# Kernel optimization log

Hardware: AMD Instinct MI355X
Metric: run time of the kernel (lower is better)

The kernel has to match this reference:

```python
import jax, jax.numpy as jnp
import numpy as np

CDIM = 32
SCALES = (1, 16, 64, 256, 1024, 4096)  # last entry == T
INV_TEMP = 100.0
ENT_W = 0.1
COMMIT_W = 0.2
Q_SCALE = 1.0 / float(np.sqrt(CDIM))


def _interp_area(x, pt):
    # x: [B, T, C] -> [B, pt, C]; T divisible by pt so 'area' == block mean
    B, T, C = x.shape
    return x.reshape(B, pt, T // pt, C).mean(axis=2)


def _interp_linear(x, T):
    # x: [B, pt, C] -> [B, T, C]; mode='linear', align_corners=False
    pt = x.shape[1]
    pos = (jnp.arange(T, dtype=jnp.float32) + 0.5) * (pt / T) - 0.5
    pos = jnp.clip(pos, 0.0, pt - 1.0)
    lo = jnp.floor(pos).astype(jnp.int32)
    hi = jnp.minimum(lo + 1, pt - 1)
    w = (pos - lo.astype(jnp.float32))[None, :, None]
    return x[:, lo] * (1.0 - w) + x[:, hi] * w


def _bsq(f):
    # L2 normalize (torch F.normalize: clamp_min on norm)
    f = f / jnp.maximum(jnp.linalg.norm(f, axis=-1, keepdims=True), 1e-12)
    # sign quantize with STE
    zhat = jnp.where(f > 0, Q_SCALE, -Q_SCALE).astype(f.dtype)
    quantized = f + jax.lax.stop_gradient(zhat - f)
    # soft entropy loss
    p = jax.nn.sigmoid(-4.0 * f * (INV_TEMP / float(np.sqrt(CDIM))))
    prob = jnp.stack([p, 1.0 - p], axis=-1)  # [B, T, C, 2]
    ent = lambda c: -(c * jnp.log(c + 1e-8)).sum(axis=-1)
    per_sample_entropy = ent(prob).sum(axis=-1).mean()
    avg_prob = prob.mean(axis=(0, 1))  # [C, 2]
    cb_entropy = ent(avg_prob).sum()
    entropy_penalty = (per_sample_entropy - cb_entropy) / INV_TEMP
    commit = ((jax.lax.stop_gradient(quantized) - f) ** 2).sum(axis=-1).mean()
    aux = entropy_penalty * ENT_W + commit * COMMIT_W
    bits = (quantized > 0).astype(jnp.int32)
    return quantized, bits, aux


def setup_inputs() -> dict:
    key = jax.random.key(0)
    B, T, C = 128, SCALES[-1], CDIM
    return {"f_BTC": jax.random.normal(key, (B, T, C), dtype=jnp.float32)}


def reference(f_BTC):
    B, T, C = f_BTC.shape
    quantized_out = jnp.zeros_like(f_BTC)
    residual = f_BTC
    losses, bit_list = [], []
    for pt in SCALES:
        interp_res = _interp_area(residual, pt) if pt != T else residual
        q, bits, loss = _bsq(interp_res)
        q = _interp_linear(q, T) if pt != T else q
        residual = residual - jax.lax.stop_gradient(q)
        quantized_out = quantized_out + q
        bit_list.append(bits)
        losses.append(loss)
    all_losses = jnp.stack(losses, axis=-1)       # [num_scales]
    all_bits = jnp.concatenate(bit_list, axis=1)  # [B, sum(SCALES), C]
    return quantized_out, all_bits, all_losses
```

## Files before the change

kernel.cpp:

```cpp
#include <hip/hip_runtime.h>
#include <hip/hip_bf16.h>
#include <cstddef>
#include <cstdint>

#define NB 128
#define NT 4096
#define NC 32
#define BITROWS 5457
#define QV_ROWS 1361
#define QOUT_ELEMS (NB*NT*NC)
#define BITS_ELEMS (NB*BITROWS*NC)

#define ACC_OFF  22298624
#define S16_OFF  22302720

__device__ __constant__ float kQSC = 0.17677669529663687f;
__device__ __constant__ float kSIG = 17.67766952966369f;

__device__ __forceinline__ float interp_slice(const float* __restrict__ q, int P, int base, int t, int c) {
  float pos = ((float)t + 0.5f) * ((float)P * (1.0f / 4096.0f)) - 0.5f;
  pos = fminf(fmaxf(pos, 0.0f), (float)(P - 1));
  const int lo = (int)pos;
  const int hi = min(lo + 1, P - 1);
  const float w = pos - (float)lo;
  const float a = __fmul_rn(q[(lo - base) * NC + c], 1.0f - w);
  const float b = __fmul_rn(q[(hi - base) * NC + c], w);
  return __fadd_rn(a, b);
}

__device__ __forceinline__ float interp_w(const float* __restrict__ plo, const float* __restrict__ phi, float w) {
  const float a = __fmul_rn(*plo, 1.0f - w);
  const float b = __fmul_rn(*phi, w);
  return __fadd_rn(a, b);
}

__device__ __forceinline__ void process_elem(
    float msum, float invn, int b, int rowOff, int j, int c,
    float* qlsRow, float* __restrict__ qvG, float* __restrict__ bitsG,
    float& entA, float& comA, float& pA)
{
  const float m = msum * invn;
  float ss = m * m;
  #pragma unroll
  for (int mk = 16; mk; mk >>= 1) ss += __shfl_xor(ss, mk, 32);
  const float den = fmaxf(sqrtf(ss), 1e-12f);
  const float fn = m / den;
  const bool bit = fn > 0.0f;
  const float zh = bit ? kQSC : -kQSC;
  const float qvv = fn + (zh - fn);
  if (qlsRow) qlsRow[c] = qvv;
  if (qvG) qvG[(size_t)b * (QV_ROWS * NC) + (size_t)(rowOff + j) * NC + c] = qvv;
  bitsG[(size_t)b * (BITROWS * NC) + (size_t)(rowOff + j) * NC + c] = bit ? 1.0f : 0.0f;
  const float arg = (-4.0f * fn) * kSIG;
  const float p = 1.0f / (1.0f + __expf(-arg));
  const float ent = -(p * __logf(p + 1e-8f) + (1.0f - p) * __logf((1.0f - p) + 1e-8f));
  const float d = qvv - fn;
  entA += ent; comA += d * d; pA += p;
}

__device__ __forceinline__ float quant_silent(float msum, float invn) {
  const float m = msum * invn;
  float ss = m * m;
  #pragma unroll
  for (int mk = 16; mk; mk >>= 1) ss += __shfl_xor(ss, mk, 32);
  const float den = fmaxf(sqrtf(ss), 1e-12f);
  const float fn = m / den;
  const float zh = (fn > 0.0f) ? kQSC : -kQSC;
  return fn + (zh - fn);
}

__device__ __forceinline__ void reduce_losses(
    int sIdx, float entA, float comA, float pA, int tid, int nWaves,
    double* __restrict__ acc, float* redE, float* redC, float* redP)
{
  float e = entA, cm = comA;
  #pragma unroll
  for (int mk = 32; mk; mk >>= 1) { e += __shfl_xor(e, mk, 64); cm += __shfl_xor(cm, mk, 64); }
  const float p = pA + __shfl_xor(pA, 32, 64);
  const int w = tid >> 6, lane = tid & 63;
  if (lane == 0) { redE[w] = e; redC[w] = cm; }
  if (lane < 32) redP[w * 32 + lane] = p;
  __syncthreads();
  if (tid == 0) {
    double te = 0.0, tc = 0.0;
    for (int i = 0; i < nWaves; ++i) { te += (double)redE[i]; tc += (double)redC[i]; }
    atomicAdd(&acc[sIdx], te);
    atomicAdd(&acc[6 + sIdx], tc);
  }
  if (tid < 32) {
    float tp = 0.0f;
    for (int i = 0; i < nWaves; ++i) tp += redP[i * 32 + tid];
    atomicAdd(&acc[12 + sIdx * 32 + tid], (double)tp);
  }
  __syncthreads();
}

__global__ __launch_bounds__(1024) void k_s0(
    const float* __restrict__ f, float* __restrict__ S16,
    float* __restrict__ qv, float* __restrict__ bitsOut, double* __restrict__ acc)
{
  __shared__ float red[1024];
  __shared__ float redE[16], redC[16], redP[16 * 32];
  const int b = blockIdx.x, tid = threadIdx.x, c = tid & 31;
  const int g = tid >> 5;
  const float* __restrict__ fbase = f + (size_t)b * (NT * NC);
  float part = 0.0f;
  #pragma unroll
  for (int j = 0; j < 8; ++j) {
    const int row = g * 8 + j;
    const float* p = fbase + (size_t)row * 16 * NC + c;
    float s = 0.0f;
    #pragma unroll
    for (int k = 0; k < 16; ++k) s += p[k * NC];
    S16[(size_t)b * 8192 + (size_t)row * NC + c] = s;
    part += s;
  }
  red[tid] = part;
  __syncthreads();
  float entA = 0.0f, comA = 0.0f, pA = 0.0f;
  if (tid < 32) {
    float msum = 0.0f;
    for (int gg = 0; gg < 32; ++gg) msum += red[gg * 32 + tid];
    process_elem(msum, 1.0f / 4096.0f, b, 0, 0, tid, nullptr, qv, bitsOut, entA, comA, pA);
  }
  reduce_losses(0, entA, comA, pA, tid, 16, acc, redE, redC, redP);
}

__global__ __launch_bounds__(1024) void k_coarse4(
    const float* __restrict__ S16g,
    float* __restrict__ qv, float* __restrict__ bitsOut, double* __restrict__ acc)
{
  __shared__ float S[96 * NC];
  __shared__ float q1s[6 * NC];
  __shared__ float q2s[18 * NC];
  __shared__ float redE[16], redC[16], redP[16 * 32];
  const int b = blockIdx.x >> 2, seg = blockIdx.x & 3;
  const int tid = threadIdx.x, c = tid & 31;
  const int s0r = 64 * seg - 16;
  const int base1 = 4 * seg - 1, base2 = 16 * seg - 1;
  const float* __restrict__ sb = S16g + (size_t)b * 8192;
  const float* __restrict__ qb = qv + (size_t)b * (QV_ROWS * NC);

  const float corr = 16.0f * qb[c];
  for (int e = tid; e < 96 * NC; e += 1024) {
    const int rw = min(max(s0r + (e >> 5), 0), 255);
    S[e] = sb[(size_t)rw * NC + (e & 31)] - corr;
  }
  __syncthreads();

  float ent, com, pp;

  ent = com = pp = 0.0f;
  if (tid < 6 * NC) {
    const int r = tid >> 5, j = base1 + r;
    if (j >= 0 && j < 16) {
      float msum = 0.0f;
      for (int jj = 0; jj < 16; ++jj) msum += S[(j * 16 + jj - s0r) * NC + c];
      if (r >= 1 && r <= 4)
        process_elem(msum, 1.0f / 256.0f, b, 1, j, c, &q1s[r * NC], qv, bitsOut, ent, com, pp);
      else
        q1s[r * NC + c] = quant_silent(msum, 1.0f / 256.0f);
    }
  }
  reduce_losses(1, ent, com, pp, tid, 16, acc, redE, redC, redP);

  for (int e = tid; e < 72 * NC; e += 1024) {
    const int g = 64 * seg - 4 + (e >> 5);
    if (g >= 0 && g < 256) {
      float cs = 0.0f;
      #pragma unroll
      for (int k = 0; k < 16; ++k) cs += interp_slice(q1s, 16, base1, g * 16 + k, c);
      S[(g - s0r) * NC + c] -= cs;
    }
  }
  __syncthreads();

  ent = com = pp = 0.0f;
  if (tid < 18 * NC) {
    const int r = tid >> 5, j2 = base2 + r;
    if (j2 >= 0 && j2 < 64) {
      float msum = 0.0f;
      #pragma unroll
      for (int jj = 0; jj < 4; ++jj) msum += S[(j2 * 4 + jj - s0r) * NC + c];
      if (r >= 1 && r <= 16)
        process_elem(msum, 1.0f / 64.0f, b, 17, j2, c, &q2s[r * NC], qv, bitsOut, ent, com, pp);
      else
        q2s[r * NC + c] = quant_silent(msum, 1.0f / 64.0f);
    }
  }
  reduce_losses(2, ent, com, pp, tid, 16, acc, redE, redC, redP);

  for (int e = tid; e < 64 * NC; e += 1024) {
    const int g = 64 * seg + (e >> 5);
    float cs = 0.0f;
    #pragma unroll
    for (int k = 0; k < 16; ++k) cs += interp_slice(q2s, 64, base2, g * 16 + k, c);
    S[(g - s0r) * NC + c] -= cs;
  }
  __syncthreads();

  ent = com = pp = 0.0f;
  for (int out = tid; out < 64 * NC; out += 1024) {
    const int g = 64 * seg + (out >> 5);
    process_elem(S[(g - s0r) * NC + c], 1.0f / 16.0f, b, 81, g, c, nullptr, qv, bitsOut, ent, com, pp);
  }
  reduce_losses(3, ent, com, pp, tid, 16, acc, redE, redC, redP);
}

__global__ __launch_bounds__(256) void k_s45(
    const float* __restrict__ f, const float* __restrict__ qv,
    float* __restrict__ qout, float* __restrict__ bitsOut, double* __restrict__ acc)
{
  __shared__ float ql0[NC];
  __shared__ float q1s[3 * NC];
  __shared__ float q2s[6 * NC];
  __shared__ float q3s[18 * NC];
  __shared__ float ql4[66 * NC];
  __shared__ float redE[4], redC[4], redP[4 * 32];
  const int b = blockIdx.x >> 4, seg = blockIdx.x & 15;
  const int tid = threadIdx.x, c = tid & 31, rloc = tid >> 5;
  const float* __restrict__ qb = qv + (size_t)b * (QV_ROWS * NC);
  const float* __restrict__ fb = f + (size_t)b * (NT * NC);
  const int b1 = seg - 1, b2 = 4 * seg - 1, b3 = 16 * seg - 1, b4 = 64 * seg - 1;
  if (tid < NC) ql0[tid] = qb[tid];
  for (int e = tid; e < 3 * NC; e += 256) {
    const int r = min(max(b1 + (e >> 5), 0), 15);
    q1s[e] = qb[(1 + r) * NC + (e & 31)];
  }
  for (int e = tid; e < 6 * NC; e += 256) {
    const int r = min(max(b2 + (e >> 5), 0), 63);
    q2s[e] = qb[(17 + r) * NC + (e & 31)];
  }
  for (int e = tid; e < 18 * NC; e += 256) {
    const int r = min(max(b3 + (e >> 5), 0), 255);
    q3s[e] = qb[(81 + r) * NC + (e & 31)];
  }
  __syncthreads();

  float entA4 = 0.0f, comA4 = 0.0f, pA4 = 0.0f;
  float entB = 0.0f, comB = 0.0f, pB = 0.0f;

  auto do_A = [&](int p, float rc[4], float qc[4]) {
    const int i = seg * 64 + p * 8 + rloc;
    const float* fp = fb + (size_t)i * 4 * NC + c;

    const bool lh1 = (i & 63) < 32;
    int rl1 = lh1 ? 0 : 1, rh1;
    float wb1 = __fmaf_rn((float)((i & 63) << 2), 0.00390625f,
                          lh1 ? 0.501953125f : -0.498046875f);
    {
      const bool cz = (seg == 0) && lh1, ch = (seg == 15) && !lh1;
      if (cz) rl1 = 1;
      rh1 = ch ? rl1 : rl1 + 1;
      if (cz || ch) wb1 = -4.0f;
    }
    const int a2r = (i >> 4) & 3;
    const bool lh2 = (i & 15) < 8;
    int rl2 = a2r + (lh2 ? 0 : 1), rh2;
    float wb2 = __fmaf_rn((float)((i & 15) << 2), 0.015625f,
                          lh2 ? 0.5078125f : -0.4921875f);
    {
      const bool cz = (seg == 0) && (a2r == 0) && lh2, ch = (seg == 15) && (a2r == 3) && !lh2;
      if (cz) rl2 = 1;
      rh2 = ch ? rl2 : rl2 + 1;
      if (cz || ch) wb2 = -4.0f;
    }
    const int a3r = (i >> 2) & 15;
    const bool lh3 = (i & 3) < 2;
    int rl3 = a3r + (lh3 ? 0 : 1), rh3;
    float wb3 = __fmaf_rn((float)((i & 3) << 2), 0.0625f,
                          lh3 ? 0.53125f : -0.46875f);
    {
      const bool cz = (seg == 0) && (a3r == 0) && lh3, ch = (seg == 15) && (a3r == 15) && !lh3;
      if (cz) rl3 = 1;
      rh3 = ch ? rl3 : rl3 + 1;
      if (cz || ch) wb3 = -4.0f;
    }
    const float* p1lo = &q1s[rl1 * NC + c]; const float* p1hi = &q1s[rh1 * NC + c];
    const float* p2lo = &q2s[rl2 * NC + c]; const float* p2hi = &q2s[rh2 * NC + c];
    const float* p3lo = &q3s[rl3 * NC + c]; const float* p3hi = &q3s[rh3 * NC + c];
    const float q0 = ql0[c];

    float msum = 0.0f;
    #pragma unroll
    for (int k = 0; k < 4; ++k) {
      float w1 = wb1 + (float)k * 0.00390625f; w1 = (w1 < 0.0f) ? 0.0f : w1;
      float w2 = wb2 + (float)k * 0.015625f;   w2 = (w2 < 0.0f) ? 0.0f : w2;
      float w3 = wb3 + (float)k * 0.0625f;     w3 = (w3 < 0.0f) ? 0.0f : w3;
      const float q1 = interp_w(p1lo, p1hi, w1);
      const float q2 = interp_w(p2lo, p2hi, w2);
      const float q3 = interp_w(p3lo, p3hi, w3);
      float r = fp[k * NC];
      r -= q0; r -= q1; r -= q2; r -= q3;
      float qs = q0; qs += q1; qs += q2; qs += q3;
      rc[k] = r; qc[k] = qs;
      msum += r;
    }
    process_elem(msum, 0.25f, b, 337, i, c,
                 &ql4[(size_t)(i - b4) * NC], nullptr, bitsOut, entA4, comA4, pA4);
  };

  auto do_halo = [&](int hr) {
    const float* fp = fb + (size_t)hr * 4 * NC + c;
    float msum = 0.0f;
    #pragma unroll
    for (int k = 0; k < 4; ++k) {
      const int t = hr * 4 + k;
      float r = fp[k * NC];
      r -= ql0[c];
      r -= interp_slice(q1s, 16,  b1, t, c);
      r -= interp_slice(q2s, 64,  b2, t, c);
      r -= interp_slice(q3s, 256, b3, t, c);
      msum += r;
    }
    ql4[(size_t)(hr - b4) * NC + c] = quant_silent(msum, 0.25f);
  };

  auto do_B = [&](int p, const float rc[4], const float qc[4]) {
    const int i = seg * 64 + p * 8 + rloc;
    const int ir = p * 8 + rloc;
    const float* r0 = &ql4[(size_t)ir * NC + c];
    const float* r1 = &ql4[(size_t)(ir + 1) * NC + c];
    const float* r2 = &ql4[(size_t)(ir + 2) * NC + c];
    const bool e0 = (i == 0), e1 = (i == 1023);
    #pragma unroll
    for (int k = 0; k < 4; ++k) {
      const float* plo; const float* phi; float w4;
      if (k < 2) {
        plo = e0 ? r1 : r0; phi = e0 ? r2 : r1;
        w4 = e0 ? 0.0f : (k == 0 ? 0.625f : 0.875f);
      } else {
        plo = r1; phi = e1 ? r1 : r2;
        w4 = e1 ? 0.0f : (k == 2 ? 0.125f : 0.375f);
      }
      const float q4 = interp_w(plo, phi, w4);
      float r = rc[k];
      r -= q4;
      float qs = qc[k];
      qs += q4;
      const int t = i * 4 + k;
      float ss = r * r;
      #pragma unroll
      for (int mk = 16; mk; mk >>= 1) ss += __shfl_xor(ss, mk, 32);
      const float den = fmaxf(sqrtf(ss), 1e-12f);
      const float fn = r / den;
      const bool bit = fn > 0.0f;
      const float zh = bit ? kQSC : -kQSC;
      const float qvv = fn + (zh - fn);
      qout[(size_t)b * (NT * NC) + (size_t)t * NC + c] = qs + qvv;
      bitsOut[(size_t)b * (BITROWS * NC) + (size_t)(1361 + t) * NC + c] = bit ? 1.0f : 0.0f;
      const float arg = (-4.0f * fn) * kSIG;
      const float p2 = 1.0f / (1.0f + __expf(-arg));
      entB += -(p2 * __logf(p2 + 1e-8f) + (1.0f - p2) * __logf((1.0f - p2) + 1e-8f));
      const float d = qvv - fn;
      comB += d * d;
      pB += p2;
    }
  };

  float rAp[4], qsAp[4];
  float rAc[4], qsAc[4];

  do_A(0, rAp, qsAp);
  if (rloc == 0 && seg > 0) do_halo(64 * seg - 1);

  for (int p = 1; p < 8; ++p) {
    do_A(p, rAc, qsAc);
    __syncthreads();
    do_B(p - 1, rAp, qsAp);
    #pragma unroll
    for (int k = 0; k < 4; ++k) { rAp[k] = rAc[k]; qsAp[k] = qsAc[k]; }
  }
  if (rloc == 1 && seg < 15) do_halo(64 * seg + 64);
  __syncthreads();
  do_B(7, rAp, qsAp);

  reduce_losses(4, entA4, comA4, pA4, tid, 4, acc, redE, redC, redP);
  reduce_losses(5, entB, comB, pB, tid, 4, acc, redE, redC, redP);
}

__global__ void k_losses(const double* __restrict__ acc, float* __restrict__ out) {
  const int s = threadIdx.x;
  if (s >= 6) return;
  const int pts[6] = {1, 16, 64, 256, 1024, 4096};
  const double n = 128.0 * (double)pts[s];
  const double pse = acc[s] / n;
  const double commit = acc[6 + s] / n;
  double cbe = 0.0;
  for (int c = 0; c < 32; ++c) {
    const double ap = acc[12 + s * 32 + c] / n;
    cbe += -(ap * log(ap + 1e-8) + (1.0 - ap) * log((1.0 - ap) + 1e-8));
  }
  const double pen = (pse - cbe) / 100.0;
  out[s] = (float)(pen * 0.1 + commit * 0.2);
}

extern "C" void kernel_launch(void* const* d_in, const int* in_sizes, int n_in,
                              void* d_out, int out_size, void* d_ws, size_t ws_size,
                              hipStream_t stream) {
  const float* f = (const float*)d_in[0];
  float* qout = (float*)d_out;
  float* bitsOut = qout + QOUT_ELEMS;
  float* lossesOut = qout + (QOUT_ELEMS + BITS_ELEMS);
  float* qv = (float*)d_ws;
  double* acc = (double*)((char*)d_ws + ACC_OFF);
  float* S16 = (float*)((char*)d_ws + S16_OFF);

  hipMemsetAsync(acc, 0, 204 * sizeof(double), stream);
  k_s0<<<NB, 1024, 0, stream>>>(f, S16, qv, bitsOut, acc);
  k_coarse4<<<NB * 4, 1024, 0, stream>>>(S16, qv, bitsOut, acc);
  k_s45<<<NB * 16, 256, 0, stream>>>(f, qv, qout, bitsOut, acc);
  k_losses<<<1, 64, 0, stream>>>(acc, lossesOut);
}
```

Baseline: 318.2 us.

## Split first-stage 16-row sums across many small blocks, move scale-0 quantize into coarse kernel

The first kernel, which used one 1024-thread block per batch, becomes a 4096-block grid of 256 threads. Each thread sums 16 rows, and each block writes a partial column sum to a scratch region of the qv workspace. The scale-1 mean, its quantization and its loss are now computed inside k_coarse4, which reads the 32 partials per batch. Only seg 0 emits bits and losses; the other segments recompute the quantized value silently. This is meant to spread the bandwidth-bound read of the input over many more CUs. The cost is redundant partial reads and a reliance on qv rows 400 onward being free scratch at that point.

```diff
diff --git a/kernel.cpp b/kernel.cpp
--- a/kernel.cpp
+++ b/kernel.cpp
@@ -13,6 +13,7 @@
 
 #define ACC_OFF  22298624
 #define S16_OFF  22302720
+#define PART_ROW 400
 
 __device__ __constant__ float kQSC = 0.17677669529663687f;
 __device__ __constant__ float kSIG = 17.67766952966369f;
@@ -95,35 +96,28 @@
   __syncthreads();
 }
 
-__global__ __launch_bounds__(1024) void k_s0(
-    const float* __restrict__ f, float* __restrict__ S16,
-    float* __restrict__ qv, float* __restrict__ bitsOut, double* __restrict__ acc)
+__global__ __launch_bounds__(256) void k_sum16p(
+    const float* __restrict__ f, float* __restrict__ S16, float* __restrict__ qv)
 {
-  __shared__ float red[1024];
-  __shared__ float redE[16], redC[16], redP[16 * 32];
-  const int b = blockIdx.x, tid = threadIdx.x, c = tid & 31;
-  const int g = tid >> 5;
-  const float* __restrict__ fbase = f + (size_t)b * (NT * NC);
-  float part = 0.0f;
+  __shared__ float sm[256];
+  const int idx = blockIdx.x * 256 + threadIdx.x;
+  const int c = idx & 31;
+  const int j = (idx >> 5) & 255;
+  const int b = idx >> 13;
+  const float* p = f + (size_t)b * (NT * NC) + (size_t)j * 16 * NC + c;
+  float s = 0.0f;
   #pragma unroll
-  for (int j = 0; j < 8; ++j) {
-    const int row = g * 8 + j;
-    const float* p = fbase + (size_t)row * 16 * NC + c;
-    float s = 0.0f;
-    #pragma unroll
-    for (int k = 0; k < 16; ++k) s += p[k * NC];
-    S16[(size_t)b * 8192 + (size_t)row * NC + c] = s;
-    part += s;
-  }
-  red[tid] = part;
-  __syncthreads();
-  float entA = 0.0f, comA = 0.0f, pA = 0.0f;
-  if (tid < 32) {
-    float msum = 0.0f;
-    for (int gg = 0; gg < 32; ++gg) msum += red[gg * 32 + tid];
-    process_elem(msum, 1.0f / 4096.0f, b, 0, 0, tid, nullptr, qv, bitsOut, entA, comA, pA);
-  }
-  reduce_losses(0, entA, comA, pA, tid, 16, acc, redE, redC, redP);
+  for (int k = 0; k < 16; ++k) s += p[k * NC];
+  S16[idx] = s;
+  sm[threadIdx.x] = s;
+  __syncthreads();
+  if (threadIdx.x < 32) {
+    float part = 0.0f;
+    #pragma unroll
+    for (int jj = 0; jj < 8; ++jj) part += sm[jj * 32 + threadIdx.x];
+    const int g = blockIdx.x & 31;
+    qv[(size_t)b * (QV_ROWS * NC) + (size_t)(PART_ROW + g) * NC + threadIdx.x] = part;
+  }
 }
 
 __global__ __launch_bounds__(1024) void k_coarse4(
@@ -133,6 +127,7 @@
   __shared__ float S[96 * NC];
   __shared__ float q1s[6 * NC];
   __shared__ float q2s[18 * NC];
+  __shared__ float sQ0[NC];
   __shared__ float redE[16], redC[16], redP[16 * 32];
   const int b = blockIdx.x >> 2, seg = blockIdx.x & 3;
   const int tid = threadIdx.x, c = tid & 31;
@@ -141,14 +136,27 @@
   const float* __restrict__ sb = S16g + (size_t)b * 8192;
   const float* __restrict__ qb = qv + (size_t)b * (QV_ROWS * NC);
 
-  const float corr = 16.0f * qb[c];
+  float ent, com, pp;
+
+  ent = com = pp = 0.0f;
+  if (tid < 32) {
+    float msum = 0.0f;
+    const float* Pw = qb + (size_t)PART_ROW * NC;
+    for (int g = 0; g < 32; ++g) msum += Pw[g * NC + tid];
+    if (seg == 0)
+      process_elem(msum, 1.0f / 4096.0f, b, 0, 0, tid, &sQ0[0], qv, bitsOut, ent, com, pp);
+    else
+      sQ0[tid] = quant_silent(msum, 1.0f / 4096.0f);
+  }
+  if (seg == 0) reduce_losses(0, ent, com, pp, tid, 16, acc, redE, redC, redP);
+  else __syncthreads();
+
+  const float corr = 16.0f * sQ0[c];
   for (int e = tid; e < 96 * NC; e += 1024) {
     const int rw = min(max(s0r + (e >> 5), 0), 255);
     S[e] = sb[(size_t)rw * NC + (e & 31)] - corr;
   }
   __syncthreads();
-
-  float ent, com, pp;
 
   ent = com = pp = 0.0f;
   if (tid < 6 * NC) {
@@ -407,7 +415,7 @@
   float* S16 = (float*)((char*)d_ws + S16_OFF);
 
   hipMemsetAsync(acc, 0, 204 * sizeof(double), stream);
-  k_s0<<<NB, 1024, 0, stream>>>(f, S16, qv, bitsOut, acc);
+  k_sum16p<<<4096, 256, 0, stream>>>(f, S16, qv);
   k_coarse4<<<NB * 4, 1024, 0, stream>>>(S16, qv, bitsOut, acc);
   k_s45<<<NB * 16, 256, 0, stream>>>(f, qv, qout, bitsOut, acc);
   k_losses<<<1, 64, 0, stream>>>(acc, lossesOut);
```

Result: slower. 326.8 us (+2.7%).
